# Kernel tuning notes

Measured on AMD Instinct MI355X. Metric: run time of the kernel, lower is better.

The kernel has to match this reference:

```python
import jax, jax.numpy as jnp
import numpy as np


def setup_inputs() -> dict:
    key = jax.random.key(0)
    k1, k2, k3 = jax.random.split(key, 3)
    B, L, D, C = 4, 4096, 1024, 1
    x = jax.random.normal(k1, (B, L, D), dtype=jnp.float32)
    kernel = jax.random.normal(k2, (C, D, L), dtype=jnp.float32)
    Dskip = jax.random.normal(k3, (C, D), dtype=jnp.float32)
    return {"x": x, "kernel": kernel, "D": Dskip}


def reference(x, kernel, D):
    # x: [B, L, H]  kernel: [C, H, L]  D: [C, H]
    L = x.shape[1]
    n = 2 * L
    xt = jnp.transpose(x, (0, 2, 1))  # [B, H, L]
    # soft-threshold the kernel: relu(|k| - 0.1) * sign(k)
    k = jax.nn.relu(jnp.abs(kernel) - 0.1) * jnp.sign(kernel)
    k_f = jnp.fft.rfft(k, n=n)          # [C, H, n//2+1] complex
    x_f = jnp.fft.rfft(xt, n=n)         # [B, H, n//2+1] complex
    y_f = jnp.einsum('bhl,chl->bchl', x_f, k_f)
    y = jnp.fft.irfft(y_f, n=n)[..., :L]            # [B, C, H, L]
    y = y + jnp.einsum('bhl,ch->bchl', xt, D)        # skip term
    # rearrange 'b c h l -> b l (c h)'
    Bn, Cn, Hn, Ln = y.shape
    return jnp.transpose(y, (0, 3, 1, 2)).reshape(Bn, Ln, Cn * Hn)
```

## Files before the change

kernel.cpp:

```cpp
#include <hip/hip_runtime.h>


typedef __attribute__((ext_vector_type(8)))  short s16x8;
typedef __attribute__((ext_vector_type(16))) float f32x16;
typedef __attribute__((ext_vector_type(4)))  float f32x4;
typedef __attribute__((ext_vector_type(4)))  unsigned int u32x4;

constexpr int B_ = 4, L_ = 4096, H_ = 1024;
constexpr int PADX = 256;
constexpr int LX = L_ + PADX;
constexpr int LK = L_ + 32;
constexpr int ST = 256;
constexpr int NST = L_ / ST;

constexpr size_t XT_ELEMS = (size_t)B_ * H_ * LX;
constexpr size_t KR_ELEMS = (size_t)2 * H_ * LK;
constexpr size_t OT_ELEMS = (size_t)B_ * H_ * L_;
constexpr size_t WS_NEEDED = (XT_ELEMS + KR_ELEMS + OT_ELEMS) * sizeof(unsigned short);

constexpr int XS_ROW  = 4320;
constexpr int XS_BLKS = XS_ROW / 8;
constexpr int XS_US   = B_ * XS_ROW;
constexpr int KS_US   = 2 * LK;
constexpr int OAREA_DW = 4 * 132;
constexpr int SMEM_BYTES = XS_US * 2 + KS_US * 2 + 4 * OAREA_DW * 4;

constexpr int nHt = H_ / 64, nLt = L_ / 64;
constexpr int NXB = B_ * nLt * nHt;

__device__ __forceinline__ unsigned short f2bf(float f) {
    unsigned int u = __builtin_bit_cast(unsigned int, f);
    u += 0x7fffu + ((u >> 16) & 1u);
    return (unsigned short)(u >> 16);
}
__device__ __forceinline__ float bf2f(unsigned short u) {
    return __builtin_bit_cast(float, (unsigned int)u << 16);
}

__global__ __launch_bounds__(256)
void prep(const float* __restrict__ x, const float* __restrict__ kin,
          const float* __restrict__ Dk,
          unsigned short* __restrict__ xT, unsigned short* __restrict__ kR)
{
    const int bid = blockIdx.x;
    if (bid < NXB) {
        __shared__ float tile[64][65];
        const int b  = bid / (nLt * nHt);
        const int r0 = bid % (nLt * nHt);
        const int l0 = (r0 / nHt) * 64;
        const int h0 = (r0 % nHt) * 64;
        const int j  = threadIdx.x;
        const int h4 = j & 15;
        const int rg = j >> 4;
        #pragma unroll
        for (int it = 0; it < 4; ++it) {
            const int lr = rg + 16 * it;
            const f32x4 v = *(const f32x4*)(x + ((size_t)b * L_ + l0 + lr) * H_ + h0 + 4 * h4);
            tile[lr][4 * h4 + 0] = v.x; tile[lr][4 * h4 + 1] = v.y;
            tile[lr][4 * h4 + 2] = v.z; tile[lr][4 * h4 + 3] = v.w;
        }
        __syncthreads();
        const int lg = j & 7;
        #pragma unroll
        for (int pp = 0; pp < 2; ++pp) {
            const int hh = (j >> 3) + 32 * pp;
            unsigned int w0 = (unsigned int)f2bf(tile[8*lg+0][hh]) | ((unsigned int)f2bf(tile[8*lg+1][hh]) << 16);
            unsigned int w1 = (unsigned int)f2bf(tile[8*lg+2][hh]) | ((unsigned int)f2bf(tile[8*lg+3][hh]) << 16);
            unsigned int w2 = (unsigned int)f2bf(tile[8*lg+4][hh]) | ((unsigned int)f2bf(tile[8*lg+5][hh]) << 16);
            unsigned int w3 = (unsigned int)f2bf(tile[8*lg+6][hh]) | ((unsigned int)f2bf(tile[8*lg+7][hh]) << 16);
            const u32x4 v = {w0, w1, w2, w3};
            *(u32x4*)(xT + ((size_t)b * H_ + h0 + hh) * LX + PADX + l0 + 8 * lg) = v;
        }
        if (l0 == 0) {
            #pragma unroll
            for (int it = 0; it < 8; ++it) {
                const int idx = j + 256 * it;
                const int row = idx >> 5, off = idx & 31;
                const u32x4 z = {};
                *(u32x4*)(xT + ((size_t)b * H_ + h0 + row) * LX + off * 8) = z;
            }
        }
    } else {
        const int h = bid - NXB;
        const float Dv = Dk[h];
        for (int l = (int)threadIdx.x; l < L_; l += 256) {
            const float a = kin[(size_t)h * L_ + l];
            float v = copysignf(fmaxf(fabsf(a) - 0.1f, 0.0f), a);
            if (l == 0) v += Dv;
            const unsigned short bv = f2bf(v);
            kR[(size_t)h * LK + (L_ - 1 - l)] = bv;
            if (l <= L_ - 2)
                kR[((size_t)H_ + h) * LK + (L_ - 2 - l)] = bv;
        }
        if (threadIdx.x < 32) kR[(size_t)h * LK + L_ + threadIdx.x] = 0;
        if (threadIdx.x < 33) kR[((size_t)H_ + h) * LK + (L_ - 1) + threadIdx.x] = 0;
    }
}

#define BODY2(M1, M2)                                                        \
  {                                                                          \
    _Pragma("unroll")                                                        \
    for (int i = 0; i < 16; ++i) {                                           \
      u32x4 aw;                                                              \
      aw.x = abase[8*i+0]; aw.y = abase[8*i+1];                              \
      aw.z = abase[8*i+2]; aw.w = abase[8*i+3];                              \
      const s16x8 af = __builtin_bit_cast(s16x8, aw);                        \
      const int io = 32 * (i >> 1);                                          \
      if (M2 >= 1) accH2 = __builtin_amdgcn_mfma_f32_32x32x16_bf16(          \
            af, held2[i], accH2, 0, 0, 0);                                   \
      if (M2 == 2) {                                                         \
        const s16x8 nf = *(const s16x8*)(((i & 1) ? p2b : p2a) + io);        \
        accL2 = __builtin_amdgcn_mfma_f32_32x32x16_bf16(af, nf, accL2,0,0,0);\
        held2[i] = nf;                                                       \
      }                                                                      \
      if (M1 >= 1) accH1 = __builtin_amdgcn_mfma_f32_32x32x16_bf16(          \
            af, held1[i], accH1, 0, 0, 0);                                   \
      if (M1 == 2) {                                                         \
        const s16x8 nf = *(const s16x8*)(((i & 1) ? p1b : p1a) + io);        \
        accL1 = __builtin_amdgcn_mfma_f32_32x32x16_bf16(af, nf, accL1,0,0,0);\
        held1[i] = nf;                                                       \
      }                                                                      \
    }                                                                        \
    abase -= 128;                                                            \
    if (M1 == 2) { p1a -= 256; p1b -= 256; }                                 \
    if (M2 == 2) { p2a -= 256; p2b -= 256; }                                 \
  }

__global__ __launch_bounds__(256, 2)
void longconv_main(const unsigned short* __restrict__ xT,
                   const unsigned short* __restrict__ kR,
                   unsigned int* __restrict__ outT)
{
    __shared__ __align__(16) unsigned char smem[SMEM_BYTES];
    unsigned short* xs = (unsigned short*)smem;
    unsigned short* ks = (unsigned short*)(smem + (size_t)XS_US * 2);
    float* oarea = (float*)(smem + (size_t)XS_US * 2 + (size_t)KS_US * 2);

    const int h   = blockIdx.x;
    const int tid = threadIdx.x;

    constexpr int NXU = XS_BLKS * 4;
    constexpr int NKU = 2 * (LK / 8);
    for (int u = tid; u < NXU + NKU; u += 256) {
        if (u < NXU) {
            const int b = u / XS_BLKS, n = u - b * XS_BLKS;
            const u32x4 v = *(const u32x4*)(xT + ((size_t)b * H_ + h) * LX + 32 + n * 8);
            *(u32x4*)(xs + (size_t)b * XS_ROW + (size_t)(n ^ b) * 8) = v;
        } else {
            const int v2 = u - NXU;
            const int p = v2 / (LK / 8), i = v2 - p * (LK / 8);
            const u32x4 v = *(const u32x4*)(kR + ((size_t)p * H_ + h) * LK + i * 8);
            *(u32x4*)(ks + (size_t)p * LK + (size_t)i * 8) = v;
        }
    }
    __syncthreads();

    const int w  = tid >> 6, ln = tid & 63;
    const int m  = ln & 31,  q  = ln >> 5;
    const int t  = m >> 2,   b  = m & 3;
    const int s1 = 2 * w;
    const int s2 = 14 - 2 * w;

    const int base = 3871 - m + 8 * q;
    const int p    = base & 1;
    const unsigned int* abase = (const unsigned int*)(ks + p * LK + (base - p));
    const unsigned short* xrow = xs + (size_t)b * XS_ROW;
    const int nb = 4 * t + q;

    auto mk = [&](int si, int par) -> const unsigned short* {
        const int n = 32 * si + nb + 2 * par;
        return xrow + (size_t)((n ^ b) * 8);
    };
    const unsigned short *p1a = mk(s1 + 1, 0), *p1b = mk(s1 + 1, 1);
    const unsigned short *p2a = mk(s2 + 1, 0), *p2b = mk(s2 + 1, 1);

    s16x8 held1[16], held2[16];
    #pragma unroll
    for (int i = 0; i < 16; ++i) {
        const int io = 32 * (i >> 1);
        held1[i] = *(const s16x8*)(((i & 1) ? p1b : p1a) + io);
        held2[i] = *(const s16x8*)(((i & 1) ? p2b : p2a) + io);
    }
    p1a -= 256; p1b -= 256; p2a -= 256; p2b -= 256;

    f32x16 accL1 = {}, accH1 = {}, accL2 = {}, accH2 = {};

    for (int beta = 0; beta <= s1; ++beta) BODY2(2, 2);
    BODY2(1, 2);
    for (int beta = s1 + 2; beta <= s2; ++beta) BODY2(0, 2);
    BODY2(0, 1);

    float* ar = oarea + w * OAREA_DW;
    auto writeout = [&](const f32x16& acc, int si) {
        const int Ls = si * ST;
        #pragma unroll
        for (int rh = 0; rh < 2; ++rh) {
            #pragma unroll
            for (int rr2 = 0; rr2 < 2; ++rr2) {
                const int base4 = (8 * rr2 + 4 * q + 4 * t) & 15;
                f32x4 qd;
                qd.x = acc[4 * (2 * rh + rr2) + 0];
                qd.y = acc[4 * (2 * rh + rr2) + 1];
                qd.z = acc[4 * (2 * rh + rr2) + 2];
                qd.w = acc[4 * (2 * rh + rr2) + 3];
                *(f32x4*)(ar + b * 132 + 16 * t + base4) = qd;
            }
            __asm__ volatile("s_waitcnt lgkmcnt(0)" ::: "memory");
            #pragma unroll
            for (int bb = 0; bb < 4; ++bb) {
                const int g  = ln >> 3;
                const int uu = (2 * ln) & 15;
                const int s  = (uu + 4 * g) & 15;
                const float v0 = ar[bb * 132 + 16 * g + s];
                const float v1 = ar[bb * 132 + 16 * g + s + 1];
                const int l = 32 * g + 16 * rh + uu;
                const unsigned int pk =
                    (unsigned int)f2bf(v0) | ((unsigned int)f2bf(v1) << 16);
                outT[(((size_t)bb * H_ + h) * L_ + Ls + l) >> 1] = pk;
            }
            __asm__ volatile("s_waitcnt lgkmcnt(0)" ::: "memory");
        }
    };
    writeout(accL1, s1);
    writeout(accH1, s1 + 1);
    writeout(accL2, s2);
    writeout(accH2, s2 + 1);
}

__global__ __launch_bounds__(256)
void untranspose(const unsigned short* __restrict__ outT, float* __restrict__ out)
{
    __shared__ float tile[64][65];
    const int bid = blockIdx.x;
    const int b  = bid / (nLt * nHt);
    const int r0 = bid % (nLt * nHt);
    const int l0 = (r0 / nHt) * 64;
    const int h0 = (r0 % nHt) * 64;
    const int j  = threadIdx.x;
    const int lg = j & 7;
    #pragma unroll
    for (int pp = 0; pp < 2; ++pp) {
        const int hh = (j >> 3) + 32 * pp;
        const u32x4 v = *(const u32x4*)(outT + ((size_t)b * H_ + h0 + hh) * L_ + l0 + 8 * lg);
        const unsigned short* pu = (const unsigned short*)&v;
        #pragma unroll
        for (int i = 0; i < 8; ++i) tile[8 * lg + i][hh] = bf2f(pu[i]);
    }
    __syncthreads();
    const int hg = j & 15;
    #pragma unroll
    for (int pp = 0; pp < 4; ++pp) {
        const int ll = (j >> 4) + 16 * pp;
        f32x4 v;
        v.x = tile[ll][4 * hg + 0];
        v.y = tile[ll][4 * hg + 1];
        v.z = tile[ll][4 * hg + 2];
        v.w = tile[ll][4 * hg + 3];
        *(f32x4*)(out + ((size_t)b * L_ + l0 + ll) * H_ + h0 + 4 * hg) = v;
    }
}

constexpr int TLf = 32, Uf = 8, Wf = TLf + Uf - 1, HTf = 256;

__global__ __launch_bounds__(HTf)
void longconv_fp32(const float* __restrict__ x, const float* __restrict__ k,
                   const float* __restrict__ Dskip, float* __restrict__ out)
{
    const int h  = blockIdx.y * HTf + threadIdx.x;
    const int b  = blockIdx.z;
    const int lt = (int)gridDim.x - 1 - (int)blockIdx.x;
    const int L0 = lt * TLf;
    const float* __restrict__ xb = x + ((size_t)b * L_) * H_ + h;
    const float* __restrict__ kh = k + (size_t)h * L_;
    float acc[TLf]; float win[Wf];
    #pragma unroll
    for (int i = 0; i < Wf; ++i) {
        const int idx = L0 - (Uf - 1) + i;
        win[i] = (idx >= 0) ? xb[(size_t)idx * H_] : 0.0f;
    }
    const float Dv = Dskip[h];
    #pragma unroll
    for (int jj = 0; jj < TLf; ++jj) acc[jj] = win[jj + Uf - 1] * Dv;
    const int cmax = L0 / Uf + (TLf / Uf) - 1;
    for (int c = 0; c <= cmax; ++c) {
        float kr[Uf];
        #pragma unroll
        for (int u = 0; u < Uf; ++u) {
            const float a = kh[c * Uf + u];
            kr[u] = copysignf(fmaxf(fabsf(a) - 0.1f, 0.0f), a);
        }
        #pragma unroll
        for (int u = 0; u < Uf; ++u)
            #pragma unroll
            for (int jj = 0; jj < TLf; ++jj)
                acc[jj] = fmaf(kr[u], win[jj + (Uf - 1) - u], acc[jj]);
        if (c < cmax) {
            #pragma unroll
            for (int i = Wf - 1; i >= Uf; --i) win[i] = win[i - Uf];
            #pragma unroll
            for (int i = 0; i < Uf; ++i) {
                const int idx = L0 - (c + 1) * Uf - (Uf - 1) + i;
                win[i] = (idx >= 0) ? xb[(size_t)idx * H_] : 0.0f;
            }
        }
    }
    float* __restrict__ ob = out + ((size_t)b * L_ + L0) * H_ + h;
    #pragma unroll
    for (int jj = 0; jj < TLf; ++jj) ob[(size_t)jj * H_] = acc[jj];
}

extern "C" void kernel_launch(void* const* d_in, const int* in_sizes, int n_in,
                              void* d_out, int out_size, void* d_ws, size_t ws_size,
                              hipStream_t stream)
{
    const float* x  = (const float*)d_in[0];
    const float* k  = (const float*)d_in[1];
    const float* Dk = (const float*)d_in[2];
    float* out = (float*)d_out;

    if (ws_size >= WS_NEEDED) {
        unsigned short* xT = (unsigned short*)d_ws;
        unsigned short* kR = xT + XT_ELEMS;
        unsigned short* oT = kR + KR_ELEMS;
        prep<<<dim3(NXB + H_), dim3(256), 0, stream>>>(x, k, Dk, xT, kR);
        longconv_main<<<dim3(H_), dim3(256), 0, stream>>>(xT, kR, (unsigned int*)oT);
        untranspose<<<dim3(NXB), dim3(256), 0, stream>>>(oT, out);
    } else {
        dim3 grid(L_ / TLf, H_ / HTf, B_);
        longconv_fp32<<<grid, dim3(HTf), 0, stream>>>(x, k, Dk, out);
    }
}
```

Measured before the change: 211.6 us.

## Vectorize kernel reversal via LDS, raise MFMA priority, swizzle untranspose tile

The kernel-prep branch now loads the soft-thresholded kernel with vector loads, stages it in shared memory, and writes the reversed bf16 rows as 16-byte stores instead of scattered 2-byte stores. The main convolution loop wraps its MFMA issue in s_setprio to favour matrix instructions across waves. The untranspose tile gets an XOR swizzle and wider rows so the read-back can use 16-byte LDS loads with fewer bank conflicts. These target the small prep and untranspose stages plus issue scheduling. They add indexing complexity and assume the padded LDS layout is correct.

```diff
diff --git a/kernel.cpp b/kernel.cpp
--- a/kernel.cpp
+++ b/kernel.cpp
@@ -36,15 +36,19 @@
 __device__ __forceinline__ float bf2f(unsigned short u) {
     return __builtin_bit_cast(float, (unsigned int)u << 16);
 }
+__device__ __forceinline__ unsigned int sw16(unsigned int x) {
+    return (x >> 16) | (x << 16);
+}
 
 __global__ __launch_bounds__(256)
 void prep(const float* __restrict__ x, const float* __restrict__ kin,
           const float* __restrict__ Dk,
           unsigned short* __restrict__ xT, unsigned short* __restrict__ kR)
 {
+    __shared__ __align__(16) unsigned char pshm[16704];
     const int bid = blockIdx.x;
     if (bid < NXB) {
-        __shared__ float tile[64][65];
+        float (*tile)[65] = (float (*)[65])pshm;
         const int b  = bid / (nLt * nHt);
         const int r0 = bid % (nLt * nHt);
         const int l0 = (r0 / nHt) * 64;
@@ -81,19 +85,51 @@
             }
         }
     } else {
+        unsigned short* kb0 = (unsigned short*)pshm;
+        unsigned short* kb1 = kb0 + 4144;
         const int h = bid - NXB;
+        const int j = threadIdx.x;
         const float Dv = Dk[h];
-        for (int l = (int)threadIdx.x; l < L_; l += 256) {
-            const float a = kin[(size_t)h * L_ + l];
-            float v = copysignf(fmaxf(fabsf(a) - 0.1f, 0.0f), a);
-            if (l == 0) v += Dv;
-            const unsigned short bv = f2bf(v);
-            kR[(size_t)h * LK + (L_ - 1 - l)] = bv;
-            if (l <= L_ - 2)
-                kR[((size_t)H_ + h) * LK + (L_ - 2 - l)] = bv;
-        }
-        if (threadIdx.x < 32) kR[(size_t)h * LK + L_ + threadIdx.x] = 0;
-        if (threadIdx.x < 33) kR[((size_t)H_ + h) * LK + (L_ - 1) + threadIdx.x] = 0;
+        if (j < 40) { kb0[j] = 0; kb1[j] = 0; }
+        const float* kh = kin + (size_t)h * L_;
+        float vv[17];
+        {
+            const int l0 = 16 * j;
+            float am = (j > 0) ? kh[l0 - 1] : 0.0f;
+            vv[0] = copysignf(fmaxf(fabsf(am) - 0.1f, 0.0f), am);
+            #pragma unroll
+            for (int g = 0; g < 4; ++g) {
+                const f32x4 a = *(const f32x4*)(kh + l0 + 4 * g);
+                vv[1 + 4*g + 0] = copysignf(fmaxf(fabsf(a.x) - 0.1f, 0.0f), a.x);
+                vv[1 + 4*g + 1] = copysignf(fmaxf(fabsf(a.y) - 0.1f, 0.0f), a.y);
+                vv[1 + 4*g + 2] = copysignf(fmaxf(fabsf(a.z) - 0.1f, 0.0f), a.z);
+                vv[1 + 4*g + 3] = copysignf(fmaxf(fabsf(a.w) - 0.1f, 0.0f), a.w);
+            }
+            if (j == 0) vv[1] += Dv;
+        }
+        {
+            unsigned int d0[8], d1[8];
+            #pragma unroll
+            for (int g = 0; g < 8; ++g) {
+                d0[g] = (unsigned int)f2bf(vv[1 + 2*g]) | ((unsigned int)f2bf(vv[2 + 2*g]) << 16);
+                d1[g] = (unsigned int)f2bf(vv[0 + 2*g]) | ((unsigned int)f2bf(vv[1 + 2*g]) << 16);
+            }
+            u32x4* p0 = (u32x4*)(kb0 + 40 + 16 * j);
+            u32x4* p1 = (u32x4*)(kb1 + 40 + 16 * j);
+            p0[0] = u32x4{d0[0], d0[1], d0[2], d0[3]};
+            p0[1] = u32x4{d0[4], d0[5], d0[6], d0[7]};
+            p1[0] = u32x4{d1[0], d1[1], d1[2], d1[3]};
+            p1[1] = u32x4{d1[4], d1[5], d1[6], d1[7]};
+        }
+        __syncthreads();
+        for (int v = j; v < LK / 8; v += 256) {
+            const u32x4 a0 = *(const u32x4*)(kb0 + 4128 - 8 * v);
+            const u32x4 a1 = *(const u32x4*)(kb1 + 4128 - 8 * v);
+            const u32x4 r0 = {sw16(a0.w), sw16(a0.z), sw16(a0.y), sw16(a0.x)};
+            const u32x4 r1 = {sw16(a1.w), sw16(a1.z), sw16(a1.y), sw16(a1.x)};
+            *(u32x4*)(kR + (size_t)h * LK + 8 * v) = r0;
+            *(u32x4*)(kR + ((size_t)H_ + h) * LK + 8 * v) = r1;
+        }
     }
 }
 
@@ -106,6 +142,7 @@
       aw.z = abase[8*i+2]; aw.w = abase[8*i+3];                              \
       const s16x8 af = __builtin_bit_cast(s16x8, aw);                        \
       const int io = 32 * (i >> 1);                                          \
+      __builtin_amdgcn_s_setprio(1);                                         \
       if (M2 >= 1) accH2 = __builtin_amdgcn_mfma_f32_32x32x16_bf16(          \
             af, held2[i], accH2, 0, 0, 0);                                   \
       if (M2 == 2) {                                                         \
@@ -120,6 +157,7 @@
         accL1 = __builtin_amdgcn_mfma_f32_32x32x16_bf16(af, nf, accL1,0,0,0);\
         held1[i] = nf;                                                       \
       }                                                                      \
+      __builtin_amdgcn_s_setprio(0);                                         \
     }                                                                        \
     abase -= 128;                                                            \
     if (M1 == 2) { p1a -= 256; p1b -= 256; }                                 \
@@ -230,7 +268,7 @@
 __global__ __launch_bounds__(256)
 void untranspose(const unsigned short* __restrict__ outT, float* __restrict__ out)
 {
-    __shared__ float tile[64][65];
+    __shared__ __align__(16) float tile[64][68];
     const int bid = blockIdx.x;
     const int b  = bid / (nLt * nHt);
     const int r0 = bid % (nLt * nHt);
@@ -244,18 +282,17 @@
         const u32x4 v = *(const u32x4*)(outT + ((size_t)b * H_ + h0 + hh) * L_ + l0 + 8 * lg);
         const unsigned short* pu = (const unsigned short*)&v;
         #pragma unroll
-        for (int i = 0; i < 8; ++i) tile[8 * lg + i][hh] = bf2f(pu[i]);
+        for (int i = 0; i < 8; ++i) {
+            const int row = 8 * lg + i;
+            tile[row][hh ^ (4 * lg)] = bf2f(pu[i]);
+        }
     }
     __syncthreads();
     const int hg = j & 15;
     #pragma unroll
     for (int pp = 0; pp < 4; ++pp) {
         const int ll = (j >> 4) + 16 * pp;
-        f32x4 v;
-        v.x = tile[ll][4 * hg + 0];
-        v.y = tile[ll][4 * hg + 1];
-        v.z = tile[ll][4 * hg + 2];
-        v.w = tile[ll][4 * hg + 3];
+        const f32x4 v = *(const f32x4*)(&tile[ll][4 * (hg ^ (ll >> 3))]);
         *(f32x4*)(out + ((size_t)b * L_ + l0 + ll) * H_ + h0 + 4 * hg) = v;
     }
 }
```

New measurement: 215.8 us. Within noise of the previous version (+2.0%).
